# Performance work log

Measured on AMD Instinct MI355X. Metric: run time of the kernel, lower is better.

The kernel has to match this reference:

```python
import jax, jax.numpy as jnp
import numpy as np
from jax.ops import segment_sum

N_NODES = 200000


def gcn_conv(x, src, dst, W, b):
    """PyG GCNConv: h = x @ W; add self-loops; symmetric deg^-1/2 norm;
    scatter-add messages to targets; add bias. Self-loop contribution is
    added analytically (norm = dinv[i]^2) instead of appending edges."""
    n = x.shape[0]
    h = x @ W                                            # [N, out]
    ones = jnp.ones(src.shape[0], dtype=x.dtype)
    deg = segment_sum(ones, dst, num_segments=n) + 1.0   # +1 for self-loop
    dinv = jax.lax.rsqrt(deg)                            # deg >= 1 always
    norm = dinv[src] * dinv[dst]                         # [E]
    agg = segment_sum(norm[:, None] * h[src], dst, num_segments=n)  # [N, out]
    return agg + (dinv * dinv)[:, None] * h + b


def setup_inputs() -> dict:
    key = jax.random.key(0)
    k1, k2, k3, k4 = jax.random.split(key, 4)
    F_in, H, C = 128, 16, 2
    x = jax.random.normal(k1, (N_NODES, F_in), dtype=jnp.float32)
    edge_index = jax.random.randint(k2, (2, 6400000), 0, N_NODES, dtype=jnp.int64)
    # Glorot-ish small weights, like torch defaults
    W1 = jax.random.normal(k3, (F_in, H), dtype=jnp.float32) / np.sqrt(F_in)
    b1 = jnp.zeros((H,), dtype=jnp.float32)
    W2 = jax.random.normal(k4, (H, C), dtype=jnp.float32) / np.sqrt(H)
    b2 = jnp.zeros((C,), dtype=jnp.float32)
    return {"x": x, "edge_index": edge_index, "W1": W1, "b1": b1, "W2": W2, "b2": b2}


def reference(x, edge_index, W1, b1, W2, b2):
    src, dst = edge_index[0], edge_index[1]
    h = gcn_conv(x, src, dst, W1, b1)
    h = jax.nn.relu(h)
    h = gcn_conv(h, src, dst, W2, b2)
    return jax.nn.log_softmax(h, axis=1)
```

## Files before the change

### kernel.cpp

```cpp
#include <hip/hip_runtime.h>
#include <math.h>

#define N_NODES 200000
#define N_EDGES 6400000
#define F_IN 128
#define NH 16
#define BKT_NODES 512
#define NB 391
#define CH 8192
#define NCHUNK 782
#define BKT_CAP 17408

#define OFF_DINV    0
#define OFF_ROW     200000
#define OFF_BCOUNT  400004
#define OFF_BBASE   400516
#define OFF_HISTB   401028
#define OFF_BASEB   801412
#define OFF_EBUF    1201796
#define OFF_H1B     7601796
#define OFF_H2B     9201796

__device__ __forceinline__ unsigned bf16rne(float f) {
    unsigned u = __float_as_uint(f);
    unsigned r = ((u >> 16) & 1u) + 0x7FFFu;
    return (u + r) >> 16;
}

__device__ __forceinline__ int detect_is32(const void* edges) {
    const long long* e64 = (const long long*)edges;
    long long v = e64[threadIdx.x & 63];
    return __any((v < 0) || (v >= N_NODES)) ? 1 : 0;
}

__global__ __launch_bounds__(512) void k_init(int* bcount) {
    bcount[threadIdx.x] = 0;
}

__global__ __launch_bounds__(256) void k_bhist(const void* edges, int* bcount,
                                               int* __restrict__ histB) {
    __shared__ int sH[512];
    int t = threadIdx.x;
    int is32 = detect_is32(edges);
    sH[t] = 0; sH[t + 256] = 0;
    __syncthreads();
    long long e0 = (long long)blockIdx.x * CH;
    int nloc = (int)min((long long)CH, (long long)N_EDGES - e0);
    int n4 = nloc >> 2;
    if (is32) {
        const int4* d4 = (const int4*)((const int*)edges + N_EDGES + e0);
        for (int j = t; j < n4; j += 256) {
            int4 d = d4[j];
            atomicAdd(&sH[d.x >> 9], 1);
            atomicAdd(&sH[d.y >> 9], 1);
            atomicAdd(&sH[d.z >> 9], 1);
            atomicAdd(&sH[d.w >> 9], 1);
        }
    } else {
        const longlong2* d2 = (const longlong2*)((const long long*)edges + N_EDGES + e0);
        for (int j = t; j < n4; j += 256) {
            longlong2 a = d2[2 * j], b = d2[2 * j + 1];
            atomicAdd(&sH[(int)a.x >> 9], 1);
            atomicAdd(&sH[(int)a.y >> 9], 1);
            atomicAdd(&sH[(int)b.x >> 9], 1);
            atomicAdd(&sH[(int)b.y >> 9], 1);
        }
    }
    __syncthreads();
    int* hb = histB + blockIdx.x * 512;
    hb[t] = sH[t];
    hb[t + 256] = sH[t + 256];
    if (sH[t]) atomicAdd(&bcount[t], sH[t]);
    if (sH[t + 256]) atomicAdd(&bcount[t + 256], sH[t + 256]);
}

__global__ __launch_bounds__(512) void k_bscan(const int* __restrict__ bcount,
                                               int* __restrict__ bbase,
                                               int* __restrict__ row_start) {
    __shared__ int sWsum[8];
    int t = threadIdx.x;
    int c = bcount[t];
    int lane = t & 63, w = t >> 6;
    int v = c;
    for (int off = 1; off < 64; off <<= 1) {
        int nbr = __shfl_up(v, off, 64);
        if (lane >= off) v += nbr;
    }
    if (lane == 63) sWsum[w] = v;
    __syncthreads();
    int add = 0;
    for (int k = 0; k < w; k++) add += sWsum[k];
    int excl = v + add - c;
    bbase[t] = excl;
    if (t == 0) row_start[N_NODES] = N_EDGES;
}

__global__ __launch_bounds__(256) void k_colscan(const int* __restrict__ histB,
                                                 const int* __restrict__ bbase,
                                                 int* __restrict__ baseB) {
    __shared__ int sW[4];
    __shared__ int sCarry;
    int q = blockIdx.x;
    int t = threadIdx.x;
    int lane = t & 63, w = t >> 6;
    if (t == 0) sCarry = bbase[q];
    __syncthreads();
    for (int c0 = 0; c0 < NCHUNK; c0 += 256) {
        int blk = c0 + t;
        int orig = (blk < NCHUNK) ? histB[blk * 512 + q] : 0;
        int v = orig;
        for (int off = 1; off < 64; off <<= 1) {
            int nbr = __shfl_up(v, off, 64);
            if (lane >= off) v += nbr;
        }
        if (lane == 63) sW[w] = v;
        __syncthreads();
        int add = sCarry;
        for (int k = 0; k < w; k++) add += sW[k];
        if (blk < NCHUNK) baseB[blk * 512 + q] = add + v - orig;
        __syncthreads();
        if (t == 255) sCarry = add + v;
        __syncthreads();
    }
}

__global__ __launch_bounds__(256) void k_bscatter(const void* edges,
                                                  const int* __restrict__ histB,
                                                  const int* __restrict__ baseB,
                                                  unsigned* __restrict__ ebuf) {
    __shared__ unsigned sS[CH];
    __shared__ int sStart[512];
    __shared__ int sCur[512];
    __shared__ int sGb[512];
    __shared__ int sWsum[4];
    int t = threadIdx.x;
    int is32 = detect_is32(edges);
    long long e0 = (long long)blockIdx.x * CH;
    int nloc = (int)min((long long)CH, (long long)N_EDGES - e0);
    int n4 = nloc >> 2;
    const int* hb = histB + blockIdx.x * 512;
    const int* bb = baseB + blockIdx.x * 512;
    int h0 = hb[2 * t], h1 = hb[2 * t + 1];
    int g0 = bb[2 * t], g1 = bb[2 * t + 1];
    int pairSum = h0 + h1;
    int lane = t & 63, w = t >> 6;
    int v = pairSum;
    for (int off = 1; off < 64; off <<= 1) {
        int nbr = __shfl_up(v, off, 64);
        if (lane >= off) v += nbr;
    }
    if (lane == 63) sWsum[w] = v;
    __syncthreads();
    int add = 0;
    for (int k = 0; k < w; k++) add += sWsum[k];
    int excl = v + add - pairSum;
    sStart[2 * t] = excl;          sStart[2 * t + 1] = excl + h0;
    sCur[2 * t] = excl;            sCur[2 * t + 1] = excl + h0;
    sGb[2 * t] = g0 - excl;        sGb[2 * t + 1] = g1 - (excl + h0);
    __syncthreads();
    if (is32) {
        const int4* s4 = (const int4*)((const int*)edges + e0);
        const int4* d4 = (const int4*)((const int*)edges + N_EDGES + e0);
        for (int j = t; j < n4; j += 256) {
            int4 s = s4[j];
            int4 d = d4[j];
            int r;
            r = atomicAdd(&sCur[d.x >> 9], 1); sS[r] = (unsigned)(((d.x & 511) << 18) | s.x);
            r = atomicAdd(&sCur[d.y >> 9], 1); sS[r] = (unsigned)(((d.y & 511) << 18) | s.y);
            r = atomicAdd(&sCur[d.z >> 9], 1); sS[r] = (unsigned)(((d.z & 511) << 18) | s.z);
            r = atomicAdd(&sCur[d.w >> 9], 1); sS[r] = (unsigned)(((d.w & 511) << 18) | s.w);
        }
    } else {
        const longlong2* s2 = (const longlong2*)((const long long*)edges + e0);
        const longlong2* d2 = (const longlong2*)((const long long*)edges + N_EDGES + e0);
        for (int j = t; j < n4; j += 256) {
            longlong2 sa = s2[2 * j], sb = s2[2 * j + 1];
            longlong2 da = d2[2 * j], db = d2[2 * j + 1];
            int s0 = (int)sa.x, s1 = (int)sa.y, s2i = (int)sb.x, s3 = (int)sb.y;
            int d0 = (int)da.x, d1 = (int)da.y, d2i = (int)db.x, d3 = (int)db.y;
            int r;
            r = atomicAdd(&sCur[d0 >> 9], 1); sS[r] = (unsigned)(((d0 & 511) << 18) | s0);
            r = atomicAdd(&sCur[d1 >> 9], 1); sS[r] = (unsigned)(((d1 & 511) << 18) | s1);
            r = atomicAdd(&sCur[d2i >> 9], 1); sS[r] = (unsigned)(((d2i & 511) << 18) | s2i);
            r = atomicAdd(&sCur[d3 >> 9], 1); sS[r] = (unsigned)(((d3 & 511) << 18) | s3);
        }
    }
    __syncthreads();
    for (int j = t; j < nloc; j += 256) {
        int lo = 0;
#pragma unroll
        for (int step = 256; step > 0; step >>= 1) {
            int mid = lo + step;
            if (mid < 512 && sStart[mid] <= j) lo = mid;
        }
        ebuf[sGb[lo] + j] = sS[j];
    }
}

__global__ __launch_bounds__(512) void k_bsort(unsigned* ebuf,
                                               const int* __restrict__ bbase,
                                               int* __restrict__ row_start,
                                               float* __restrict__ dinv) {
    __shared__ unsigned sE[BKT_CAP];
    __shared__ int sH[512];
    __shared__ int sWsum[8];
    int b = blockIdx.x, t = threadIdx.x;
    int base = bbase[b];
    int cnt = bbase[b + 1] - base;
    int cap = cnt < BKT_CAP ? cnt : BKT_CAP;
    for (int j = t; j < cap; j += 512) sE[j] = ebuf[base + j];
    sH[t] = 0;
    __syncthreads();
    for (int j = t; j < cnt; j += 512) {
        unsigned p = (j < cap) ? sE[j] : ebuf[base + j];
        atomicAdd(&sH[p >> 18], 1);
    }
    __syncthreads();
    int h = sH[t];
    int lane = t & 63, w = t >> 6;
    int v = h;
    for (int off = 1; off < 64; off <<= 1) {
        int nbr = __shfl_up(v, off, 64);
        if (lane >= off) v += nbr;
    }
    if (lane == 63) sWsum[w] = v;
    __syncthreads();
    int add = 0;
    for (int k = 0; k < w; k++) add += sWsum[k];
    int excl = v + add - h;
    int node = b * BKT_NODES + t;
    if (node < N_NODES) {
        row_start[node] = base + excl;
        dinv[node] = rsqrtf((float)h + 1.0f);
    }
    __syncthreads();
    sH[t] = excl;
    __syncthreads();
    for (int j = t; j < cnt; j += 512) {
        unsigned p = (j < cap) ? sE[j] : ebuf[base + j];
        int pos = atomicAdd(&sH[p >> 18], 1);
        ebuf[base + pos] = p & 0x3FFFF;
    }
}

__global__ __launch_bounds__(256) void k_gemm1(const float* __restrict__ x,
                                               const float* __restrict__ W1,
                                               const float* __restrict__ dinv,
                                               unsigned short* __restrict__ h1b) {
    __shared__ float sWt[NH * F_IN];
    int t = threadIdx.x;
    for (int q = t; q < 512; q += 256) {
        float4 wv = ((const float4*)W1)[q];
        int k = q >> 2, c0 = (q & 3) * 4;
        sWt[(c0 + 0) * F_IN + k] = wv.x;
        sWt[(c0 + 1) * F_IN + k] = wv.y;
        sWt[(c0 + 2) * F_IN + k] = wv.z;
        sWt[(c0 + 3) * F_IN + k] = wv.w;
    }
    __syncthreads();
    int r = blockIdx.x * 64 + (t >> 2);
    int l = t & 3;
    if (r >= N_NODES) return;
    float acc[NH];
#pragma unroll
    for (int c = 0; c < NH; c++) acc[c] = 0.f;
    const float4* xr = (const float4*)(x + (size_t)r * F_IN);
#pragma unroll
    for (int s = 0; s < 8; s++) {
        float4 xv = xr[s * 4 + l];
        int k0 = s * 16 + l * 4;
#pragma unroll
        for (int c = 0; c < NH; c++) {
            float4 wv = *(const float4*)&sWt[c * F_IN + k0];
            acc[c] += xv.x * wv.x + xv.y * wv.y + xv.z * wv.z + xv.w * wv.w;
        }
    }
#pragma unroll
    for (int c = 0; c < NH; c++) {
        acc[c] += __shfl_xor(acc[c], 1, 4);
        acc[c] += __shfl_xor(acc[c], 2, 4);
    }
    float di = dinv[r];
    unsigned p0 = bf16rne(acc[l * 4 + 0] * di) | (bf16rne(acc[l * 4 + 1] * di) << 16);
    unsigned p1 = bf16rne(acc[l * 4 + 2] * di) | (bf16rne(acc[l * 4 + 3] * di) << 16);
    *(uint2*)(h1b + (size_t)r * NH + l * 4) = make_uint2(p0, p1);
}

__global__ __launch_bounds__(256) void k_gather1(const int* __restrict__ row_start,
                                                 const int* __restrict__ csr_src,
                                                 const float* __restrict__ dinv,
                                                 const unsigned short* __restrict__ h1b,
                                                 const float* __restrict__ b1,
                                                 const float* __restrict__ W2,
                                                 float* __restrict__ h2b) {
    int t = threadIdx.x;
    int i = blockIdx.x * 16 + (t >> 4);
    int fq = t & 3;
    int slot = (t >> 2) & 3;
    int start = row_start[i];
    int end = row_start[i + 1];
    float di = dinv[i];
    float4 acc = make_float4(0.f, 0.f, 0.f, 0.f);
    for (int e = start + slot; e < end; e += 4) {
        int src = csr_src[e];
        uint2 v = *(const uint2*)(h1b + ((size_t)src << 4) + (fq << 2));
        acc.x += __uint_as_float(v.x << 16);
        acc.y += __uint_as_float(v.x & 0xFFFF0000u);
        acc.z += __uint_as_float(v.y << 16);
        acc.w += __uint_as_float(v.y & 0xFFFF0000u);
    }
    acc.x += __shfl_xor(acc.x, 4, 16);
    acc.y += __shfl_xor(acc.y, 4, 16);
    acc.z += __shfl_xor(acc.z, 4, 16);
    acc.w += __shfl_xor(acc.w, 4, 16);
    acc.x += __shfl_xor(acc.x, 8, 16);
    acc.y += __shfl_xor(acc.y, 8, 16);
    acc.z += __shfl_xor(acc.z, 8, 16);
    acc.w += __shfl_xor(acc.w, 8, 16);
    float v0 = 0.f, v1 = 0.f;
    if (slot == 0) {
        uint2 sv = *(const uint2*)(h1b + ((size_t)i << 4) + (fq << 2));
        float s0 = __uint_as_float(sv.x << 16);
        float s1 = __uint_as_float(sv.x & 0xFFFF0000u);
        float s2 = __uint_as_float(sv.y << 16);
        float s3 = __uint_as_float(sv.y & 0xFFFF0000u);
        int f0 = fq << 2;
        float r0 = fmaxf(di * (acc.x + s0) + b1[f0 + 0], 0.f);
        float r1 = fmaxf(di * (acc.y + s1) + b1[f0 + 1], 0.f);
        float r2 = fmaxf(di * (acc.z + s2) + b1[f0 + 2], 0.f);
        float r3 = fmaxf(di * (acc.w + s3) + b1[f0 + 3], 0.f);
        v0 = r0 * W2[(f0 + 0) * 2] + r1 * W2[(f0 + 1) * 2] +
             r2 * W2[(f0 + 2) * 2] + r3 * W2[(f0 + 3) * 2];
        v1 = r0 * W2[(f0 + 0) * 2 + 1] + r1 * W2[(f0 + 1) * 2 + 1] +
             r2 * W2[(f0 + 2) * 2 + 1] + r3 * W2[(f0 + 3) * 2 + 1];
        v0 += __shfl_xor(v0, 1, 4);
        v1 += __shfl_xor(v1, 1, 4);
        v0 += __shfl_xor(v0, 2, 4);
        v1 += __shfl_xor(v1, 2, 4);
        if (fq == 0) {
            float2 hv;
            hv.x = di * v0;
            hv.y = di * v1;
            *(float2*)(h2b + (size_t)i * 2) = hv;
        }
    }
}

__global__ __launch_bounds__(256) void k_gather2(const int* __restrict__ row_start,
                                                 const int* __restrict__ csr_src,
                                                 const float* __restrict__ dinv,
                                                 const float* __restrict__ h2b,
                                                 const float* __restrict__ b2,
                                                 float* __restrict__ out) {
    int t = threadIdx.x;
    int i = blockIdx.x * 64 + (t >> 2);
    int l = t & 3;
    int start = row_start[i];
    int end = row_start[i + 1];
    float di = dinv[i];
    float o0 = 0.f, o1 = 0.f;
    for (int e = start + l; e < end; e += 4) {
        int src = csr_src[e];
        float2 hv = *(const float2*)(h2b + (size_t)src * 2);
        o0 += hv.x;
        o1 += hv.y;
    }
    o0 += __shfl_xor(o0, 1, 4);
    o1 += __shfl_xor(o1, 1, 4);
    o0 += __shfl_xor(o0, 2, 4);
    o1 += __shfl_xor(o1, 2, 4);
    if (l == 0) {
        float2 hs = *(const float2*)(h2b + (size_t)i * 2);
        float f0 = di * (o0 + hs.x) + b2[0];
        float f1 = di * (o1 + hs.y) + b2[1];
        float m = fmaxf(f0, f1);
        float lse = m + logf(expf(f0 - m) + expf(f1 - m));
        out[(size_t)i * 2 + 0] = f0 - lse;
        out[(size_t)i * 2 + 1] = f1 - lse;
    }
}

extern "C" void kernel_launch(void* const* d_in, const int* in_sizes, int n_in,
                              void* d_out, int out_size, void* d_ws, size_t ws_size,
                              hipStream_t stream) {
    const float* x  = (const float*)d_in[0];
    const void*  ei = d_in[1];
    const float* W1 = (const float*)d_in[2];
    const float* b1 = (const float*)d_in[3];
    const float* W2 = (const float*)d_in[4];
    const float* b2 = (const float*)d_in[5];

    int*            wsw       = (int*)d_ws;
    float*          dinv      = (float*)(wsw + OFF_DINV);
    int*            row_start = wsw + OFF_ROW;
    int*            bcount    = wsw + OFF_BCOUNT;
    int*            bbase     = wsw + OFF_BBASE;
    int*            histB     = wsw + OFF_HISTB;
    int*            baseB     = wsw + OFF_BASEB;
    unsigned*       ebuf      = (unsigned*)(wsw + OFF_EBUF);
    unsigned short* h1b       = (unsigned short*)(wsw + OFF_H1B);
    float*          h2b       = (float*)(wsw + OFF_H2B);
    float*          out       = (float*)d_out;

    k_init<<<1, 512, 0, stream>>>(bcount);
    k_bhist<<<NCHUNK, 256, 0, stream>>>(ei, bcount, histB);
    k_bscan<<<1, 512, 0, stream>>>(bcount, bbase, row_start);
    k_colscan<<<512, 256, 0, stream>>>(histB, bbase, baseB);
    k_bscatter<<<NCHUNK, 256, 0, stream>>>(ei, histB, baseB, ebuf);
    k_bsort<<<NB, 512, 0, stream>>>(ebuf, bbase, row_start, dinv);
    k_gemm1<<<(N_NODES + 63) / 64, 256, 0, stream>>>(x, W1, dinv, h1b);
    k_gather1<<<N_NODES / 16, 256, 0, stream>>>(row_start, (const int*)ebuf, dinv, h1b, b1, W2, h2b);
    k_gather2<<<N_NODES / 64, 256, 0, stream>>>(row_start, (const int*)ebuf, dinv, h2b, b2, out);
}
```

Baseline: 256.8 us.

## Split layer-1 features into two halves and gather each in a separate pass

The bf16 hidden features are split into two 8-feature arrays (each 3.2 MB instead of one 6.4 MB array). The layer-1 gather runs twice, once per half, so each pass's random-access working set is smaller and more likely to stay in the L2/last-level cache. The first pass stores partial layer-2 projections and the second combines them. The cost is reading the CSR index array twice, an extra kernel launch, and an extra partial buffer round trip.

Result: slower. 269.8 us (+5.0%).

```diff
diff --git a/kernel.cpp b/kernel.cpp
--- a/kernel.cpp
+++ b/kernel.cpp
@@ -18,8 +18,10 @@
 #define OFF_HISTB   401028
 #define OFF_BASEB   801412
 #define OFF_EBUF    1201796
-#define OFF_H1B     7601796
-#define OFF_H2B     9201796
+#define OFF_H1BA    7601796
+#define OFF_H1BB    8401796
+#define OFF_H2P     9201796
+#define OFF_H2B     9601796
 
 __device__ __forceinline__ unsigned bf16rne(float f) {
     unsigned u = __float_as_uint(f);
@@ -246,7 +248,8 @@
 __global__ __launch_bounds__(256) void k_gemm1(const float* __restrict__ x,
                                                const float* __restrict__ W1,
                                                const float* __restrict__ dinv,
-                                               unsigned short* __restrict__ h1b) {
+                                               unsigned short* __restrict__ h1bA,
+                                               unsigned short* __restrict__ h1bB) {
     __shared__ float sWt[NH * F_IN];
     int t = threadIdx.x;
     for (int q = t; q < 512; q += 256) {
@@ -283,32 +286,39 @@
     float di = dinv[r];
     unsigned p0 = bf16rne(acc[l * 4 + 0] * di) | (bf16rne(acc[l * 4 + 1] * di) << 16);
     unsigned p1 = bf16rne(acc[l * 4 + 2] * di) | (bf16rne(acc[l * 4 + 3] * di) << 16);
-    *(uint2*)(h1b + (size_t)r * NH + l * 4) = make_uint2(p0, p1);
-}
-
-__global__ __launch_bounds__(256) void k_gather1(const int* __restrict__ row_start,
-                                                 const int* __restrict__ csr_src,
-                                                 const float* __restrict__ dinv,
-                                                 const unsigned short* __restrict__ h1b,
-                                                 const float* __restrict__ b1,
-                                                 const float* __restrict__ W2,
-                                                 float* __restrict__ h2b) {
+    unsigned short* dst = (l < 2) ? h1bA : h1bB;
+    *(uint2*)(dst + ((size_t)r << 3) + ((l & 1) << 2)) = make_uint2(p0, p1);
+}
+
+__global__ __launch_bounds__(256) void k_gather1h(const int* __restrict__ row_start,
+                                                  const int* __restrict__ csr_src,
+                                                  const float* __restrict__ dinv,
+                                                  const unsigned short* __restrict__ h1bX,
+                                                  const float* __restrict__ b1,
+                                                  const float* __restrict__ W2,
+                                                  float* __restrict__ h2p,
+                                                  float* __restrict__ h2b,
+                                                  int phase) {
     int t = threadIdx.x;
     int i = blockIdx.x * 16 + (t >> 4);
-    int fq = t & 3;
-    int slot = (t >> 2) & 3;
+    int q = t & 1;
+    int slot = (t >> 1) & 7;
     int start = row_start[i];
     int end = row_start[i + 1];
     float di = dinv[i];
     float4 acc = make_float4(0.f, 0.f, 0.f, 0.f);
-    for (int e = start + slot; e < end; e += 4) {
+    for (int e = start + slot; e < end; e += 8) {
         int src = csr_src[e];
-        uint2 v = *(const uint2*)(h1b + ((size_t)src << 4) + (fq << 2));
+        uint2 v = *(const uint2*)(h1bX + ((size_t)src << 3) + (q << 2));
         acc.x += __uint_as_float(v.x << 16);
         acc.y += __uint_as_float(v.x & 0xFFFF0000u);
         acc.z += __uint_as_float(v.y << 16);
         acc.w += __uint_as_float(v.y & 0xFFFF0000u);
     }
+    acc.x += __shfl_xor(acc.x, 2, 16);
+    acc.y += __shfl_xor(acc.y, 2, 16);
+    acc.z += __shfl_xor(acc.z, 2, 16);
+    acc.w += __shfl_xor(acc.w, 2, 16);
     acc.x += __shfl_xor(acc.x, 4, 16);
     acc.y += __shfl_xor(acc.y, 4, 16);
     acc.z += __shfl_xor(acc.z, 4, 16);
@@ -317,31 +327,33 @@
     acc.y += __shfl_xor(acc.y, 8, 16);
     acc.z += __shfl_xor(acc.z, 8, 16);
     acc.w += __shfl_xor(acc.w, 8, 16);
-    float v0 = 0.f, v1 = 0.f;
     if (slot == 0) {
-        uint2 sv = *(const uint2*)(h1b + ((size_t)i << 4) + (fq << 2));
+        uint2 sv = *(const uint2*)(h1bX + ((size_t)i << 3) + (q << 2));
         float s0 = __uint_as_float(sv.x << 16);
         float s1 = __uint_as_float(sv.x & 0xFFFF0000u);
         float s2 = __uint_as_float(sv.y << 16);
         float s3 = __uint_as_float(sv.y & 0xFFFF0000u);
-        int f0 = fq << 2;
+        int f0 = phase * 8 + q * 4;
         float r0 = fmaxf(di * (acc.x + s0) + b1[f0 + 0], 0.f);
         float r1 = fmaxf(di * (acc.y + s1) + b1[f0 + 1], 0.f);
         float r2 = fmaxf(di * (acc.z + s2) + b1[f0 + 2], 0.f);
         float r3 = fmaxf(di * (acc.w + s3) + b1[f0 + 3], 0.f);
-        v0 = r0 * W2[(f0 + 0) * 2] + r1 * W2[(f0 + 1) * 2] +
-             r2 * W2[(f0 + 2) * 2] + r3 * W2[(f0 + 3) * 2];
-        v1 = r0 * W2[(f0 + 0) * 2 + 1] + r1 * W2[(f0 + 1) * 2 + 1] +
-             r2 * W2[(f0 + 2) * 2 + 1] + r3 * W2[(f0 + 3) * 2 + 1];
-        v0 += __shfl_xor(v0, 1, 4);
-        v1 += __shfl_xor(v1, 1, 4);
-        v0 += __shfl_xor(v0, 2, 4);
-        v1 += __shfl_xor(v1, 2, 4);
-        if (fq == 0) {
-            float2 hv;
-            hv.x = di * v0;
-            hv.y = di * v1;
-            *(float2*)(h2b + (size_t)i * 2) = hv;
+        float p0 = r0 * W2[(f0 + 0) * 2] + r1 * W2[(f0 + 1) * 2] +
+                   r2 * W2[(f0 + 2) * 2] + r3 * W2[(f0 + 3) * 2];
+        float p1 = r0 * W2[(f0 + 0) * 2 + 1] + r1 * W2[(f0 + 1) * 2 + 1] +
+                   r2 * W2[(f0 + 2) * 2 + 1] + r3 * W2[(f0 + 3) * 2 + 1];
+        p0 += __shfl_xor(p0, 1, 2);
+        p1 += __shfl_xor(p1, 1, 2);
+        if (q == 0) {
+            if (phase == 0) {
+                h2p[(size_t)i * 2 + 0] = p0;
+                h2p[(size_t)i * 2 + 1] = p1;
+            } else {
+                float2 hv;
+                hv.x = di * (h2p[(size_t)i * 2 + 0] + p0);
+                hv.y = di * (h2p[(size_t)i * 2 + 1] + p1);
+                *(float2*)(h2b + (size_t)i * 2) = hv;
+            }
         }
     }
 }
@@ -398,7 +410,9 @@
     int*            histB     = wsw + OFF_HISTB;
     int*            baseB     = wsw + OFF_BASEB;
     unsigned*       ebuf      = (unsigned*)(wsw + OFF_EBUF);
-    unsigned short* h1b       = (unsigned short*)(wsw + OFF_H1B);
+    unsigned short* h1bA      = (unsigned short*)(wsw + OFF_H1BA);
+    unsigned short* h1bB      = (unsigned short*)(wsw + OFF_H1BB);
+    float*          h2p       = (float*)(wsw + OFF_H2P);
     float*          h2b       = (float*)(wsw + OFF_H2B);
     float*          out       = (float*)d_out;
 
@@ -408,7 +422,8 @@
     k_colscan<<<512, 256, 0, stream>>>(histB, bbase, baseB);
     k_bscatter<<<NCHUNK, 256, 0, stream>>>(ei, histB, baseB, ebuf);
     k_bsort<<<NB, 512, 0, stream>>>(ebuf, bbase, row_start, dinv);
-    k_gemm1<<<(N_NODES + 63) / 64, 256, 0, stream>>>(x, W1, dinv, h1b);
-    k_gather1<<<N_NODES / 16, 256, 0, stream>>>(row_start, (const int*)ebuf, dinv, h1b, b1, W2, h2b);
+    k_gemm1<<<(N_NODES + 63) / 64, 256, 0, stream>>>(x, W1, dinv, h1bA, h1bB);
+    k_gather1h<<<N_NODES / 16, 256, 0, stream>>>(row_start, (const int*)ebuf, dinv, h1bA, b1, W2, h2p, h2b, 0);
+    k_gather1h<<<N_NODES / 16, 256, 0, stream>>>(row_start, (const int*)ebuf, dinv, h1bB, b1, W2, h2p, h2b, 1);
     k_gather2<<<N_NODES / 64, 256, 0, stream>>>(row_start, (const int*)ebuf, dinv, h2b, b2, out);
 }
```

## Drop per-bucket CSR sort; aggregate bucketed edges via shared-memory atomics

Applied to the files above, without the earlier changes.

Replaces the full in-bucket counting sort that built a CSR with bucket-only grouping of 256 destination nodes. A light degree kernel replaces the sort, and both gather kernels now stream each bucket's edges and accumulate messages into shared-memory float atomics before the per-node epilogue. This removes one full read/write pass over the edge buffer. In exchange each edge costs 16 (or 2) LDS float atomics, bucket-level parallelism is coarser, and the bin count doubles to 1024 in the histogram and scatter stages.

After: 861.1 us. 235% more time.

```diff
diff --git a/kernel.cpp b/kernel.cpp
--- a/kernel.cpp
+++ b/kernel.cpp
@@ -5,27 +5,27 @@
 #define N_EDGES 6400000
 #define F_IN 128
 #define NH 16
-#define BKT_NODES 512
-#define NB 391
+#define BKT_NODES 256
+#define NBINS 1024
+#define NB 782
 #define CH 8192
 #define NCHUNK 782
-#define BKT_CAP 17408
 
 #define OFF_DINV    0
-#define OFF_ROW     200000
-#define OFF_BCOUNT  400004
-#define OFF_BBASE   400516
-#define OFF_HISTB   401028
-#define OFF_BASEB   801412
-#define OFF_EBUF    1201796
-#define OFF_H1B     7601796
-#define OFF_H2B     9201796
+#define OFF_BCOUNT  200000
+#define OFF_BBASE   201024
+#define OFF_HISTB   202048
+#define OFF_BASEB   1002816
+#define OFF_EBUF    1803584
+#define OFF_H1B     8203584
+#define OFF_H2B     9803584
 
 __device__ __forceinline__ unsigned bf16rne(float f) {
     unsigned u = __float_as_uint(f);
     unsigned r = ((u >> 16) & 1u) + 0x7FFFu;
     return (u + r) >> 16;
 }
+__device__ __forceinline__ float uaf(unsigned u) { return __uint_as_float(u); }
 
 __device__ __forceinline__ int detect_is32(const void* edges) {
     const long long* e64 = (const long long*)edges;
@@ -33,55 +33,55 @@
     return __any((v < 0) || (v >= N_NODES)) ? 1 : 0;
 }
 
-__global__ __launch_bounds__(512) void k_init(int* bcount) {
+__global__ __launch_bounds__(1024) void k_init(int* bcount) {
     bcount[threadIdx.x] = 0;
 }
 
-__global__ __launch_bounds__(256) void k_bhist(const void* edges, int* bcount,
+__global__ __launch_bounds__(512) void k_bhist(const void* edges, int* bcount,
                                                int* __restrict__ histB) {
-    __shared__ int sH[512];
+    __shared__ int sH[NBINS];
     int t = threadIdx.x;
     int is32 = detect_is32(edges);
-    sH[t] = 0; sH[t + 256] = 0;
+    sH[t] = 0; sH[t + 512] = 0;
     __syncthreads();
     long long e0 = (long long)blockIdx.x * CH;
     int nloc = (int)min((long long)CH, (long long)N_EDGES - e0);
     int n4 = nloc >> 2;
     if (is32) {
         const int4* d4 = (const int4*)((const int*)edges + N_EDGES + e0);
-        for (int j = t; j < n4; j += 256) {
+        for (int j = t; j < n4; j += 512) {
             int4 d = d4[j];
-            atomicAdd(&sH[d.x >> 9], 1);
-            atomicAdd(&sH[d.y >> 9], 1);
-            atomicAdd(&sH[d.z >> 9], 1);
-            atomicAdd(&sH[d.w >> 9], 1);
+            atomicAdd(&sH[d.x >> 8], 1);
+            atomicAdd(&sH[d.y >> 8], 1);
+            atomicAdd(&sH[d.z >> 8], 1);
+            atomicAdd(&sH[d.w >> 8], 1);
         }
     } else {
         const longlong2* d2 = (const longlong2*)((const long long*)edges + N_EDGES + e0);
-        for (int j = t; j < n4; j += 256) {
+        for (int j = t; j < n4; j += 512) {
             longlong2 a = d2[2 * j], b = d2[2 * j + 1];
-            atomicAdd(&sH[(int)a.x >> 9], 1);
-            atomicAdd(&sH[(int)a.y >> 9], 1);
-            atomicAdd(&sH[(int)b.x >> 9], 1);
-            atomicAdd(&sH[(int)b.y >> 9], 1);
-        }
-    }
-    __syncthreads();
-    int* hb = histB + blockIdx.x * 512;
+            atomicAdd(&sH[(int)a.x >> 8], 1);
+            atomicAdd(&sH[(int)a.y >> 8], 1);
+            atomicAdd(&sH[(int)b.x >> 8], 1);
+            atomicAdd(&sH[(int)b.y >> 8], 1);
+        }
+    }
+    __syncthreads();
+    int* hb = histB + blockIdx.x * NBINS;
     hb[t] = sH[t];
-    hb[t + 256] = sH[t + 256];
+    hb[t + 512] = sH[t + 512];
     if (sH[t]) atomicAdd(&bcount[t], sH[t]);
-    if (sH[t + 256]) atomicAdd(&bcount[t + 256], sH[t + 256]);
+    if (sH[t + 512]) atomicAdd(&bcount[t + 512], sH[t + 512]);
 }
 
 __global__ __launch_bounds__(512) void k_bscan(const int* __restrict__ bcount,
-                                               int* __restrict__ bbase,
-                                               int* __restrict__ row_start) {
+                                               int* __restrict__ bbase) {
     __shared__ int sWsum[8];
     int t = threadIdx.x;
-    int c = bcount[t];
+    int c0 = bcount[2 * t], c1 = bcount[2 * t + 1];
+    int pairSum = c0 + c1;
     int lane = t & 63, w = t >> 6;
-    int v = c;
+    int v = pairSum;
     for (int off = 1; off < 64; off <<= 1) {
         int nbr = __shfl_up(v, off, 64);
         if (lane >= off) v += nbr;
@@ -90,9 +90,9 @@
     __syncthreads();
     int add = 0;
     for (int k = 0; k < w; k++) add += sWsum[k];
-    int excl = v + add - c;
-    bbase[t] = excl;
-    if (t == 0) row_start[N_NODES] = N_EDGES;
+    int excl = v + add - pairSum;
+    bbase[2 * t] = excl;
+    bbase[2 * t + 1] = excl + c0;
 }
 
 __global__ __launch_bounds__(256) void k_colscan(const int* __restrict__ histB,
@@ -107,7 +107,7 @@
     __syncthreads();
     for (int c0 = 0; c0 < NCHUNK; c0 += 256) {
         int blk = c0 + t;
-        int orig = (blk < NCHUNK) ? histB[blk * 512 + q] : 0;
+        int orig = (blk < NCHUNK) ? histB[blk * NBINS + q] : 0;
         int v = orig;
         for (int off = 1; off < 64; off <<= 1) {
             int nbr = __shfl_up(v, off, 64);
@@ -117,29 +117,29 @@
         __syncthreads();
         int add = sCarry;
         for (int k = 0; k < w; k++) add += sW[k];
-        if (blk < NCHUNK) baseB[blk * 512 + q] = add + v - orig;
+        if (blk < NCHUNK) baseB[blk * NBINS + q] = add + v - orig;
         __syncthreads();
         if (t == 255) sCarry = add + v;
         __syncthreads();
     }
 }
 
-__global__ __launch_bounds__(256) void k_bscatter(const void* edges,
+__global__ __launch_bounds__(512) void k_bscatter(const void* edges,
                                                   const int* __restrict__ histB,
                                                   const int* __restrict__ baseB,
                                                   unsigned* __restrict__ ebuf) {
     __shared__ unsigned sS[CH];
-    __shared__ int sStart[512];
-    __shared__ int sCur[512];
-    __shared__ int sGb[512];
-    __shared__ int sWsum[4];
+    __shared__ int sStart[NBINS];
+    __shared__ int sCur[NBINS];
+    __shared__ int sGb[NBINS];
+    __shared__ int sWsum[8];
     int t = threadIdx.x;
     int is32 = detect_is32(edges);
     long long e0 = (long long)blockIdx.x * CH;
     int nloc = (int)min((long long)CH, (long long)N_EDGES - e0);
     int n4 = nloc >> 2;
-    const int* hb = histB + blockIdx.x * 512;
-    const int* bb = baseB + blockIdx.x * 512;
+    const int* hb = histB + blockIdx.x * NBINS;
+    const int* bb = baseB + blockIdx.x * NBINS;
     int h0 = hb[2 * t], h1 = hb[2 * t + 1];
     int g0 = bb[2 * t], g1 = bb[2 * t + 1];
     int pairSum = h0 + h1;
@@ -161,85 +161,57 @@
     if (is32) {
         const int4* s4 = (const int4*)((const int*)edges + e0);
         const int4* d4 = (const int4*)((const int*)edges + N_EDGES + e0);
-        for (int j = t; j < n4; j += 256) {
+        for (int j = t; j < n4; j += 512) {
             int4 s = s4[j];
             int4 d = d4[j];
             int r;
-            r = atomicAdd(&sCur[d.x >> 9], 1); sS[r] = (unsigned)(((d.x & 511) << 18) | s.x);
-            r = atomicAdd(&sCur[d.y >> 9], 1); sS[r] = (unsigned)(((d.y & 511) << 18) | s.y);
-            r = atomicAdd(&sCur[d.z >> 9], 1); sS[r] = (unsigned)(((d.z & 511) << 18) | s.z);
-            r = atomicAdd(&sCur[d.w >> 9], 1); sS[r] = (unsigned)(((d.w & 511) << 18) | s.w);
+            r = atomicAdd(&sCur[d.x >> 8], 1); sS[r] = (unsigned)(((d.x & 255) << 18) | s.x);
+            r = atomicAdd(&sCur[d.y >> 8], 1); sS[r] = (unsigned)(((d.y & 255) << 18) | s.y);
+            r = atomicAdd(&sCur[d.z >> 8], 1); sS[r] = (unsigned)(((d.z & 255) << 18) | s.z);
+            r = atomicAdd(&sCur[d.w >> 8], 1); sS[r] = (unsigned)(((d.w & 255) << 18) | s.w);
         }
     } else {
         const longlong2* s2 = (const longlong2*)((const long long*)edges + e0);
         const longlong2* d2 = (const longlong2*)((const long long*)edges + N_EDGES + e0);
-        for (int j = t; j < n4; j += 256) {
+        for (int j = t; j < n4; j += 512) {
             longlong2 sa = s2[2 * j], sb = s2[2 * j + 1];
             longlong2 da = d2[2 * j], db = d2[2 * j + 1];
             int s0 = (int)sa.x, s1 = (int)sa.y, s2i = (int)sb.x, s3 = (int)sb.y;
             int d0 = (int)da.x, d1 = (int)da.y, d2i = (int)db.x, d3 = (int)db.y;
             int r;
-            r = atomicAdd(&sCur[d0 >> 9], 1); sS[r] = (unsigned)(((d0 & 511) << 18) | s0);
-            r = atomicAdd(&sCur[d1 >> 9], 1); sS[r] = (unsigned)(((d1 & 511) << 18) | s1);
-            r = atomicAdd(&sCur[d2i >> 9], 1); sS[r] = (unsigned)(((d2i & 511) << 18) | s2i);
-            r = atomicAdd(&sCur[d3 >> 9], 1); sS[r] = (unsigned)(((d3 & 511) << 18) | s3);
-        }
-    }
-    __syncthreads();
-    for (int j = t; j < nloc; j += 256) {
+            r = atomicAdd(&sCur[d0 >> 8], 1); sS[r] = (unsigned)(((d0 & 255) << 18) | s0);
+            r = atomicAdd(&sCur[d1 >> 8], 1); sS[r] = (unsigned)(((d1 & 255) << 18) | s1);
+            r = atomicAdd(&sCur[d2i >> 8], 1); sS[r] = (unsigned)(((d2i & 255) << 18) | s2i);
+            r = atomicAdd(&sCur[d3 >> 8], 1); sS[r] = (unsigned)(((d3 & 255) << 18) | s3);
+        }
+    }
+    __syncthreads();
+    for (int j = t; j < nloc; j += 512) {
         int lo = 0;
 #pragma unroll
-        for (int step = 256; step > 0; step >>= 1) {
+        for (int step = 512; step > 0; step >>= 1) {
             int mid = lo + step;
-            if (mid < 512 && sStart[mid] <= j) lo = mid;
+            if (mid < NBINS && sStart[mid] <= j) lo = mid;
         }
         ebuf[sGb[lo] + j] = sS[j];
     }
 }
 
-__global__ __launch_bounds__(512) void k_bsort(unsigned* ebuf,
-                                               const int* __restrict__ bbase,
-                                               int* __restrict__ row_start,
-                                               float* __restrict__ dinv) {
-    __shared__ unsigned sE[BKT_CAP];
-    __shared__ int sH[512];
-    __shared__ int sWsum[8];
+__global__ __launch_bounds__(512) void k_degb(const unsigned* __restrict__ ebuf,
+                                              const int* __restrict__ bbase,
+                                              float* __restrict__ dinv) {
+    __shared__ int sCnt[BKT_NODES];
     int b = blockIdx.x, t = threadIdx.x;
     int base = bbase[b];
     int cnt = bbase[b + 1] - base;
-    int cap = cnt < BKT_CAP ? cnt : BKT_CAP;
-    for (int j = t; j < cap; j += 512) sE[j] = ebuf[base + j];
-    sH[t] = 0;
-    __syncthreads();
-    for (int j = t; j < cnt; j += 512) {
-        unsigned p = (j < cap) ? sE[j] : ebuf[base + j];
-        atomicAdd(&sH[p >> 18], 1);
-    }
-    __syncthreads();
-    int h = sH[t];
-    int lane = t & 63, w = t >> 6;
-    int v = h;
-    for (int off = 1; off < 64; off <<= 1) {
-        int nbr = __shfl_up(v, off, 64);
-        if (lane >= off) v += nbr;
-    }
-    if (lane == 63) sWsum[w] = v;
-    __syncthreads();
-    int add = 0;
-    for (int k = 0; k < w; k++) add += sWsum[k];
-    int excl = v + add - h;
-    int node = b * BKT_NODES + t;
-    if (node < N_NODES) {
-        row_start[node] = base + excl;
-        dinv[node] = rsqrtf((float)h + 1.0f);
-    }
-    __syncthreads();
-    sH[t] = excl;
-    __syncthreads();
-    for (int j = t; j < cnt; j += 512) {
-        unsigned p = (j < cap) ? sE[j] : ebuf[base + j];
-        int pos = atomicAdd(&sH[p >> 18], 1);
-        ebuf[base + pos] = p & 0x3FFFF;
+    if (t < BKT_NODES) sCnt[t] = 0;
+    __syncthreads();
+    for (int j = t; j < cnt; j += 512)
+        atomicAdd(&sCnt[ebuf[base + j] >> 18], 1);
+    __syncthreads();
+    if (t < BKT_NODES) {
+        int node = b * BKT_NODES + t;
+        if (node < N_NODES) dinv[node] = rsqrtf((float)sCnt[t] + 1.0f);
     }
 }
 
@@ -286,97 +258,121 @@
     *(uint2*)(h1b + (size_t)r * NH + l * 4) = make_uint2(p0, p1);
 }
 
-__global__ __launch_bounds__(256) void k_gather1(const int* __restrict__ row_start,
-                                                 const int* __restrict__ csr_src,
-                                                 const float* __restrict__ dinv,
-                                                 const unsigned short* __restrict__ h1b,
-                                                 const float* __restrict__ b1,
-                                                 const float* __restrict__ W2,
-                                                 float* __restrict__ h2b) {
-    int t = threadIdx.x;
-    int i = blockIdx.x * 16 + (t >> 4);
-    int fq = t & 3;
-    int slot = (t >> 2) & 3;
-    int start = row_start[i];
-    int end = row_start[i + 1];
-    float di = dinv[i];
-    float4 acc = make_float4(0.f, 0.f, 0.f, 0.f);
-    for (int e = start + slot; e < end; e += 4) {
-        int src = csr_src[e];
-        uint2 v = *(const uint2*)(h1b + ((size_t)src << 4) + (fq << 2));
-        acc.x += __uint_as_float(v.x << 16);
-        acc.y += __uint_as_float(v.x & 0xFFFF0000u);
-        acc.z += __uint_as_float(v.y << 16);
-        acc.w += __uint_as_float(v.y & 0xFFFF0000u);
-    }
-    acc.x += __shfl_xor(acc.x, 4, 16);
-    acc.y += __shfl_xor(acc.y, 4, 16);
-    acc.z += __shfl_xor(acc.z, 4, 16);
-    acc.w += __shfl_xor(acc.w, 4, 16);
-    acc.x += __shfl_xor(acc.x, 8, 16);
-    acc.y += __shfl_xor(acc.y, 8, 16);
-    acc.z += __shfl_xor(acc.z, 8, 16);
-    acc.w += __shfl_xor(acc.w, 8, 16);
-    float v0 = 0.f, v1 = 0.f;
-    if (slot == 0) {
-        uint2 sv = *(const uint2*)(h1b + ((size_t)i << 4) + (fq << 2));
-        float s0 = __uint_as_float(sv.x << 16);
-        float s1 = __uint_as_float(sv.x & 0xFFFF0000u);
-        float s2 = __uint_as_float(sv.y << 16);
-        float s3 = __uint_as_float(sv.y & 0xFFFF0000u);
-        int f0 = fq << 2;
-        float r0 = fmaxf(di * (acc.x + s0) + b1[f0 + 0], 0.f);
-        float r1 = fmaxf(di * (acc.y + s1) + b1[f0 + 1], 0.f);
-        float r2 = fmaxf(di * (acc.z + s2) + b1[f0 + 2], 0.f);
-        float r3 = fmaxf(di * (acc.w + s3) + b1[f0 + 3], 0.f);
-        v0 = r0 * W2[(f0 + 0) * 2] + r1 * W2[(f0 + 1) * 2] +
-             r2 * W2[(f0 + 2) * 2] + r3 * W2[(f0 + 3) * 2];
-        v1 = r0 * W2[(f0 + 0) * 2 + 1] + r1 * W2[(f0 + 1) * 2 + 1] +
-             r2 * W2[(f0 + 2) * 2 + 1] + r3 * W2[(f0 + 3) * 2 + 1];
-        v0 += __shfl_xor(v0, 1, 4);
-        v1 += __shfl_xor(v1, 1, 4);
-        v0 += __shfl_xor(v0, 2, 4);
-        v1 += __shfl_xor(v1, 2, 4);
-        if (fq == 0) {
+__device__ __forceinline__ void acc_edge(float* row, uint4 lo, uint4 hi) {
+    atomicAdd(row + 0,  uaf(lo.x << 16)); atomicAdd(row + 1,  uaf(lo.x & 0xFFFF0000u));
+    atomicAdd(row + 2,  uaf(lo.y << 16)); atomicAdd(row + 3,  uaf(lo.y & 0xFFFF0000u));
+    atomicAdd(row + 4,  uaf(lo.z << 16)); atomicAdd(row + 5,  uaf(lo.z & 0xFFFF0000u));
+    atomicAdd(row + 6,  uaf(lo.w << 16)); atomicAdd(row + 7,  uaf(lo.w & 0xFFFF0000u));
+    atomicAdd(row + 8,  uaf(hi.x << 16)); atomicAdd(row + 9,  uaf(hi.x & 0xFFFF0000u));
+    atomicAdd(row + 10, uaf(hi.y << 16)); atomicAdd(row + 11, uaf(hi.y & 0xFFFF0000u));
+    atomicAdd(row + 12, uaf(hi.z << 16)); atomicAdd(row + 13, uaf(hi.z & 0xFFFF0000u));
+    atomicAdd(row + 14, uaf(hi.w << 16)); atomicAdd(row + 15, uaf(hi.w & 0xFFFF0000u));
+}
+
+__global__ __launch_bounds__(512) void k_gather1f(const unsigned* __restrict__ ebuf,
+                                                  const int* __restrict__ bbase,
+                                                  const float* __restrict__ dinv,
+                                                  const unsigned short* __restrict__ h1b,
+                                                  const float* __restrict__ b1,
+                                                  const float* __restrict__ W2,
+                                                  float* __restrict__ h2b) {
+    __shared__ float sAgg[BKT_NODES * 17];
+    int b = blockIdx.x, t = threadIdx.x;
+    int base = bbase[b];
+    int cnt = bbase[b + 1] - base;
+    for (int j = t; j < BKT_NODES * 17; j += 512) sAgg[j] = 0.f;
+    __syncthreads();
+    int j = t;
+    for (; j + 512 < cnt; j += 1024) {
+        unsigned p0 = ebuf[base + j];
+        unsigned p1 = ebuf[base + j + 512];
+        const uint4* hp0 = (const uint4*)(h1b + ((size_t)(p0 & 0x3FFFF) << 4));
+        const uint4* hp1 = (const uint4*)(h1b + ((size_t)(p1 & 0x3FFFF) << 4));
+        uint4 lo0 = hp0[0], hi0 = hp0[1];
+        uint4 lo1 = hp1[0], hi1 = hp1[1];
+        acc_edge(&sAgg[(p0 >> 18) * 17], lo0, hi0);
+        acc_edge(&sAgg[(p1 >> 18) * 17], lo1, hi1);
+    }
+    for (; j < cnt; j += 512) {
+        unsigned p = ebuf[base + j];
+        const uint4* hp = (const uint4*)(h1b + ((size_t)(p & 0x3FFFF) << 4));
+        uint4 lo = hp[0], hi = hp[1];
+        acc_edge(&sAgg[(p >> 18) * 17], lo, hi);
+    }
+    __syncthreads();
+    if (t < BKT_NODES) {
+        int node = b * BKT_NODES + t;
+        if (node < N_NODES) {
+            float di = dinv[node];
+            const uint4* hp = (const uint4*)(h1b + ((size_t)node << 4));
+            uint4 lo = hp[0], hi = hp[1];
+            float sf[16];
+            sf[0] = uaf(lo.x << 16);  sf[1] = uaf(lo.x & 0xFFFF0000u);
+            sf[2] = uaf(lo.y << 16);  sf[3] = uaf(lo.y & 0xFFFF0000u);
+            sf[4] = uaf(lo.z << 16);  sf[5] = uaf(lo.z & 0xFFFF0000u);
+            sf[6] = uaf(lo.w << 16);  sf[7] = uaf(lo.w & 0xFFFF0000u);
+            sf[8] = uaf(hi.x << 16);  sf[9] = uaf(hi.x & 0xFFFF0000u);
+            sf[10] = uaf(hi.y << 16); sf[11] = uaf(hi.y & 0xFFFF0000u);
+            sf[12] = uaf(hi.z << 16); sf[13] = uaf(hi.z & 0xFFFF0000u);
+            sf[14] = uaf(hi.w << 16); sf[15] = uaf(hi.w & 0xFFFF0000u);
+            const float* a = &sAgg[t * 17];
+            float p0 = 0.f, p1 = 0.f;
+#pragma unroll
+            for (int f = 0; f < 16; f++) {
+                float rv = fmaxf(di * (a[f] + sf[f]) + b1[f], 0.f);
+                p0 += rv * W2[f * 2 + 0];
+                p1 += rv * W2[f * 2 + 1];
+            }
             float2 hv;
-            hv.x = di * v0;
-            hv.y = di * v1;
-            *(float2*)(h2b + (size_t)i * 2) = hv;
-        }
-    }
-}
-
-__global__ __launch_bounds__(256) void k_gather2(const int* __restrict__ row_start,
-                                                 const int* __restrict__ csr_src,
-                                                 const float* __restrict__ dinv,
-                                                 const float* __restrict__ h2b,
-                                                 const float* __restrict__ b2,
-                                                 float* __restrict__ out) {
-    int t = threadIdx.x;
-    int i = blockIdx.x * 64 + (t >> 2);
-    int l = t & 3;
-    int start = row_start[i];
-    int end = row_start[i + 1];
-    float di = dinv[i];
-    float o0 = 0.f, o1 = 0.f;
-    for (int e = start + l; e < end; e += 4) {
-        int src = csr_src[e];
-        float2 hv = *(const float2*)(h2b + (size_t)src * 2);
-        o0 += hv.x;
-        o1 += hv.y;
-    }
-    o0 += __shfl_xor(o0, 1, 4);
-    o1 += __shfl_xor(o1, 1, 4);
-    o0 += __shfl_xor(o0, 2, 4);
-    o1 += __shfl_xor(o1, 2, 4);
-    if (l == 0) {
-        float2 hs = *(const float2*)(h2b + (size_t)i * 2);
-        float f0 = di * (o0 + hs.x) + b2[0];
-        float f1 = di * (o1 + hs.y) + b2[1];
-        float m = fmaxf(f0, f1);
-        float lse = m + logf(expf(f0 - m) + expf(f1 - m));
-        out[(size_t)i * 2 + 0] = f0 - lse;
-        out[(size_t)i * 2 + 1] = f1 - lse;
+            hv.x = di * p0;
+            hv.y = di * p1;
+            *(float2*)(h2b + (size_t)node * 2) = hv;
+        }
+    }
+}
+
+__global__ __launch_bounds__(512) void k_gather2f(const unsigned* __restrict__ ebuf,
+                                                  const int* __restrict__ bbase,
+                                                  const float* __restrict__ dinv,
+                                                  const float* __restrict__ h2b,
+                                                  const float* __restrict__ b2,
+                                                  float* __restrict__ out) {
+    __shared__ float sA[BKT_NODES * 3];
+    int b = blockIdx.x, t = threadIdx.x;
+    int base = bbase[b];
+    int cnt = bbase[b + 1] - base;
+    for (int j = t; j < BKT_NODES * 3; j += 512) sA[j] = 0.f;
+    __syncthreads();
+    int j = t;
+    for (; j + 512 < cnt; j += 1024) {
+        unsigned p0 = ebuf[base + j];
+        unsigned p1 = ebuf[base + j + 512];
+        float2 h0 = *(const float2*)(h2b + ((size_t)(p0 & 0x3FFFF) << 1));
+        float2 h1 = *(const float2*)(h2b + ((size_t)(p1 & 0x3FFFF) << 1));
+        atomicAdd(&sA[(p0 >> 18) * 3 + 0], h0.x);
+        atomicAdd(&sA[(p0 >> 18) * 3 + 1], h0.y);
+        atomicAdd(&sA[(p1 >> 18) * 3 + 0], h1.x);
+        atomicAdd(&sA[(p1 >> 18) * 3 + 1], h1.y);
+    }
+    for (; j < cnt; j += 512) {
+        unsigned p = ebuf[base + j];
+        float2 hv = *(const float2*)(h2b + ((size_t)(p & 0x3FFFF) << 1));
+        atomicAdd(&sA[(p >> 18) * 3 + 0], hv.x);
+        atomicAdd(&sA[(p >> 18) * 3 + 1], hv.y);
+    }
+    __syncthreads();
+    if (t < BKT_NODES) {
+        int node = b * BKT_NODES + t;
+        if (node < N_NODES) {
+            float di = dinv[node];
+            float2 hs = *(const float2*)(h2b + (size_t)node * 2);
+            float f0 = di * (sA[t * 3 + 0] + hs.x) + b2[0];
+            float f1 = di * (sA[t * 3 + 1] + hs.y) + b2[1];
+            float m = fmaxf(f0, f1);
+            float lse = m + logf(expf(f0 - m) + expf(f1 - m));
+            out[(size_t)node * 2 + 0] = f0 - lse;
+            out[(size_t)node * 2 + 1] = f1 - lse;
+        }
     }
 }
 
@@ -392,7 +388,6 @@
 
     int*            wsw       = (int*)d_ws;
     float*          dinv      = (float*)(wsw + OFF_DINV);
-    int*            row_start = wsw + OFF_ROW;
     int*            bcount    = wsw + OFF_BCOUNT;
     int*            bbase     = wsw + OFF_BBASE;
     int*            histB     = wsw + OFF_HISTB;
@@ -402,13 +397,13 @@
     float*          h2b       = (float*)(wsw + OFF_H2B);
     float*          out       = (float*)d_out;
 
-    k_init<<<1, 512, 0, stream>>>(bcount);
-    k_bhist<<<NCHUNK, 256, 0, stream>>>(ei, bcount, histB);
-    k_bscan<<<1, 512, 0, stream>>>(bcount, bbase, row_start);
-    k_colscan<<<512, 256, 0, stream>>>(histB, bbase, baseB);
-    k_bscatter<<<NCHUNK, 256, 0, stream>>>(ei, histB, baseB, ebuf);
-    k_bsort<<<NB, 512, 0, stream>>>(ebuf, bbase, row_start, dinv);
+    k_init<<<1, 1024, 0, stream>>>(bcount);
+    k_bhist<<<NCHUNK, 512, 0, stream>>>(ei, bcount, histB);
+    k_bscan<<<1, 512, 0, stream>>>(bcount, bbase);
+    k_colscan<<<NBINS, 256, 0, stream>>>(histB, bbase, baseB);
+    k_bscatter<<<NCHUNK, 512, 0, stream>>>(ei, histB, baseB, ebuf);
+    k_degb<<<NB, 512, 0, stream>>>(ebuf, bbase, dinv);
     k_gemm1<<<(N_NODES + 63) / 64, 256, 0, stream>>>(x, W1, dinv, h1b);
-    k_gather1<<<N_NODES / 16, 256, 0, stream>>>(row_start, (const int*)ebuf, dinv, h1b, b1, W2, h2b);
-    k_gather2<<<N_NODES / 64, 256, 0, stream>>>(row_start, (const int*)ebuf, dinv, h2b, b2, out);
-}
+    k_gather1f<<<NB, 512, 0, stream>>>(ebuf, bbase, dinv, h1b, b1, W2, h2b);
+    k_gather2f<<<NB, 512, 0, stream>>>(ebuf, bbase, dinv, h2b, b2, out);
+}
```
